# Kernel optimization log

Hardware: AMD Instinct MI355X
Metric: run time of the kernel (lower is better)

## Reference

```python
import jax, jax.numpy as jnp
import numpy as np

B, N, E_PER = 32, 2048, 16384
DIN, H = 128, 128
RATIO = 0.3


def setup_inputs() -> dict:
    key = jax.random.key(0)
    ks = jax.random.split(key, 16)
    s_in = 1.0 / np.sqrt(DIN)
    s_h = 1.0 / np.sqrt(H)
    inp = {
        "x": jax.random.normal(ks[0], (B * N, DIN), dtype=jnp.float32),
        "edge_src": jax.random.randint(ks[1], (B, E_PER), 0, N, dtype=jnp.int32),
        "edge_dst": jax.random.randint(ks[2], (B, E_PER), 0, N, dtype=jnp.int32),
        # SAGEConv layer 1: lin_l (neighbor agg, with bias), lin_r (root, no bias)
        "Wl1": jax.random.normal(ks[3], (H, DIN), dtype=jnp.float32) * s_in,
        "bl1": jnp.zeros((H,), dtype=jnp.float32),
        "Wr1": jax.random.normal(ks[4], (H, DIN), dtype=jnp.float32) * s_in,
        # SAGEConv layer 2
        "Wl2": jax.random.normal(ks[5], (H, H), dtype=jnp.float32) * s_h,
        "bl2": jnp.zeros((H,), dtype=jnp.float32),
        "Wr2": jax.random.normal(ks[6], (H, H), dtype=jnp.float32) * s_h,
        # TopKPooling score weight
        "pool_w": jax.random.normal(ks[7], (H,), dtype=jnp.float32) * s_h,
        # classifier MLP
        "Wc1": jax.random.normal(ks[8], (H, H), dtype=jnp.float32) * s_h,
        "bc1": jnp.zeros((H,), dtype=jnp.float32),
        "Wc2": jax.random.normal(ks[9], (1, H), dtype=jnp.float32) * s_h,
        "bc2": jnp.zeros((1,), dtype=jnp.float32),
    }
    return inp


def _sage_conv(x, src, dst, n_total, Wl, bl, Wr):
    # mean-aggregate neighbor messages: msg flows src -> dst
    msg = x[src]                                                   # [E, D] gather
    agg = jax.ops.segment_sum(msg, dst, num_segments=n_total)      # [Nt, D]
    deg = jax.ops.segment_sum(jnp.ones_like(dst, dtype=x.dtype), dst,
                              num_segments=n_total)
    agg = agg / jnp.maximum(deg, 1.0)[:, None]
    return agg @ Wl.T + bl + x @ Wr.T


def _forward(x, edge_src, edge_dst, Wl1, bl1, Wr1, Wl2, bl2, Wr2,
             pool_w, Wc1, bc1, Wc2, bc2):
    n_total = x.shape[0]
    # offset per-graph node ids into the disjoint-union batch
    off = (jnp.arange(B, dtype=edge_src.dtype) * N)[:, None]
    src = (edge_src + off).reshape(-1)
    dst = (edge_dst + off).reshape(-1)

    x = jax.nn.relu(_sage_conv(x, src, dst, n_total, Wl1, bl1, Wr1))
    x = jax.nn.relu(_sage_conv(x, src, dst, n_total, Wl2, bl2, Wr2))

    # TopKPooling: score = tanh(x . w / ||w||); keep top ceil(ratio*N) per graph
    score = jnp.tanh(x @ pool_w / jnp.linalg.norm(pool_w))         # [Nt]
    k = int(np.ceil(RATIO * N))                                    # 615
    vals, idx = jax.lax.top_k(score.reshape(B, N), k)              # [B, k]
    xg = x.reshape(B, N, -1)
    x_sel = jnp.take_along_axis(xg, idx[..., None], axis=1)        # [B, k, H]
    x_sel = x_sel * vals[..., None]                                # gate by score

    # global mean pool over kept nodes, then MLP classifier
    emb = x_sel.mean(axis=1)                                       # [B, H]
    h = jax.nn.relu(emb @ Wc1.T + bc1)
    return (h @ Wc2.T + bc2).squeeze(-1)                           # [B]


def reference(x, edge_src, edge_dst, Wl1, bl1, Wr1, Wl2, bl2, Wr2,
              pool_w, Wc1, bc1, Wc2, bc2):
    return _forward(x, edge_src, edge_dst, Wl1, bl1, Wr1, Wl2, bl2, Wr2,
                    pool_w, Wc1, bc1, Wc2, bc2)
```

## Files before the change

kernel.cpp:

```cpp
#include <hip/hip_runtime.h>
#include <stdint.h>
#include <math.h>

#define NB    32
#define NNODE 2048
#define NT    (NB*NNODE)
#define EPB   16384
#define ETOT  (NB*EPB)
#define DF    128
#define KSEL  615
#define EMAX  512

typedef __attribute__((ext_vector_type(8))) short bf16x8;
typedef __attribute__((ext_vector_type(4))) float f32x4;

__device__ __forceinline__ unsigned short f2bf(float f){
  uint32_t u = __float_as_uint(f);
  u += 0x7FFFu + ((u>>16)&1u);
  return (unsigned short)(u>>16);
}
__device__ __forceinline__ void split2(float f, unsigned short& hi, unsigned short& lo){
  unsigned short h = f2bf(f);
  float fh = __uint_as_float(((uint32_t)h)<<16);
  hi = h;
  lo = f2bf(f - fh);
}
__device__ __forceinline__ uint32_t f2mono(float f){
  uint32_t u = __float_as_uint(f);
  return (u & 0x80000000u) ? ~u : (u | 0x80000000u);
}
__device__ __forceinline__ float mono2f(uint32_t m){
  uint32_t u = (m & 0x80000000u) ? (m ^ 0x80000000u) : ~m;
  return __uint_as_float(u);
}

__global__ void k_deg(const int* __restrict__ edst, uint32_t* __restrict__ deg,
                      const float* __restrict__ Wl1, const float* __restrict__ Wr1,
                      const float* __restrict__ Wl2, const float* __restrict__ Wr2,
                      unsigned short* __restrict__ Bpk){
  const int bid = blockIdx.x;
  if (bid < ETOT/256){
    int e = bid*256 + threadIdx.x;
    int g = e >> 14;
    atomicAdd(&deg[g*NNODE + edst[e]], 1u);
  } else {
    int tt = (bid - ETOT/256)*256 + threadIdx.x;
    int layer = tt >> 12;
    int t2 = tt & 4095;
    const float* Wl = layer ? Wl2 : Wl1;
    const float* Wr = layer ? Wr2 : Wr1;
    unsigned short* B = Bpk + (size_t)layer*65536;
    int lane = t2 & 63;
    int ct   = (t2>>6) & 7;
    int ks   = (t2>>9) & 7;
    int c  = ct*16 + (lane & 15);
    int k0 = ks*32 + ((lane>>4)<<3);
    size_t base = ((size_t)((ks*8+ct)*2)*64 + lane)*8;
    #pragma unroll
    for (int j=0;j<8;++j){
      int k = k0 + j;
      float v = (k < DF) ? Wl[c*DF + k] : Wr[c*DF + (k-DF)];
      unsigned short h, l; split2(v, h, l);
      B[base + j]       = h;
      B[base + 512 + j] = l;
    }
  }
}

__global__ __launch_bounds__(1024) void k_scan1(const uint32_t* __restrict__ deg,
                        uint32_t* __restrict__ rowptr, uint32_t* __restrict__ bsum){
  __shared__ uint32_t sh[1024];
  int t = threadIdx.x; int base = blockIdx.x*1024;
  uint32_t v = deg[base+t];
  sh[t] = v;
  for (int off=1; off<1024; off<<=1){
    __syncthreads();
    uint32_t a = (t>=off) ? sh[t-off] : 0u;
    __syncthreads();
    sh[t] += a;
  }
  rowptr[base+t] = sh[t] - v;
  if (t==1023) bsum[blockIdx.x] = sh[1023];
}

__global__ void k_scan2(uint32_t* __restrict__ bsum){
  __shared__ uint32_t sh[64];
  int t = threadIdx.x;
  uint32_t v = bsum[t]; sh[t] = v;
  for (int off=1; off<64; off<<=1){
    __syncthreads();
    uint32_t a = (t>=off) ? sh[t-off] : 0u;
    __syncthreads();
    sh[t] += a;
  }
  bsum[t] = sh[t] - v;
}

__global__ __launch_bounds__(1024) void k_scan3(uint32_t* __restrict__ rowptr,
                                                const uint32_t* __restrict__ bsum){
  int i = blockIdx.x*1024 + threadIdx.x;
  rowptr[i] += bsum[i>>10];
  if (i==0) rowptr[NT] = ETOT;
}

__global__ void k_scatter(const int* __restrict__ esrc, const int* __restrict__ edst,
                          const uint32_t* __restrict__ rowptr, uint32_t* __restrict__ deg,
                          int* __restrict__ col){
  int e = blockIdx.x*256 + threadIdx.x;
  int g = e >> 14;
  int d = g*NNODE + edst[e];
  int s = g*NNODE + esrc[e];
  uint32_t old = atomicSub(&deg[d], 1u);
  col[rowptr[d] + old - 1u] = s;
}

template<int LAYER>
__global__ __launch_bounds__(128, 4) void k_sage(
    const float* __restrict__ Xin, const uint32_t* __restrict__ rowptr,
    const int* __restrict__ col, const unsigned short* __restrict__ Bpk,
    const float* __restrict__ bias, float* __restrict__ OUT,
    const float* __restrict__ pw, float* __restrict__ scores)
{
  __shared__ float smemA[32][132];
  __shared__ int lcol[EMAX];
  __shared__ uint32_t lrpl[33];

  const int t = threadIdx.x;
  const int g = blockIdx.x & 31, jb = blockIdx.x >> 5;
  const int rowBase = g*NNODE + jb*32;

  const uint32_t e0 = rowptr[rowBase];
  if (t < 33) lrpl[t] = rowptr[rowBase + t] - e0;
  const int ecnt = (int)(rowptr[rowBase + 32] - e0);
  for (int i=t; i<ecnt && i<EMAX; i+=128) lcol[i] = col[e0+i];
  __syncthreads();

  {
    const int grp = t >> 5, c = t & 31;
    int cur = grp*8;
    const int curEnd = grp*8 + 8;
    f32x4 accv = {0.f,0.f,0.f,0.f};

    auto flushrow = [&](){
      uint32_t d = lrpl[cur+1] - lrpl[cur];
      float invd = 1.0f / (float)(d ? d : 1u);
      *(f32x4*)&smemA[cur][4*c] = accv * invd;
      accv = (f32x4){0.f,0.f,0.f,0.f};
      cur++;
    };

    const uint32_t kb = lrpl[grp*8], ke = lrpl[curEnd];
    auto run = [&](auto colAt){
      f32x4 v[8], w[8];
      #pragma unroll
      for (int j=0;j<8;++j){
        uint32_t kk = kb + j;
        int s = colAt(kk < ke ? kk : kb);
        v[j] = *(const f32x4*)(Xin + (size_t)s*DF + 4*c);
      }
      for (uint32_t k = kb; k < ke; k += 8){
        #pragma unroll
        for (int j=0;j<8;++j){
          uint32_t kk = k + 8 + j;
          int s = colAt(kk < ke ? kk : k);
          w[j] = *(const f32x4*)(Xin + (size_t)s*DF + 4*c);
        }
        #pragma unroll
        for (int j=0;j<8;++j){
          uint32_t kk = k + j;
          if (kk < ke){
            while (lrpl[cur+1] <= kk) flushrow();
            accv += v[j];
          }
        }
        #pragma unroll
        for (int j=0;j<8;++j) v[j] = w[j];
      }
    };
    if (kb < ke){
      if (ecnt <= EMAX) run([&](uint32_t k){ return lcol[k]; });
      else              run([&](uint32_t k){ return col[e0+k]; });
    }
    while (cur < curEnd) flushrow();
  }
  __syncthreads();

  const int l = t & 63, wid = t >> 6;
  const int q = l >> 4, c16 = l & 15;
  const int arow = rowBase + wid*16 + c16;

  f32x4 own[8];
  #pragma unroll
  for (int ks4=0; ks4<4; ++ks4){
    const float* s = Xin + (size_t)arow*DF + ks4*32 + q*8;
    own[ks4*2]   = *(const f32x4*)s;
    own[ks4*2+1] = *(const f32x4*)(s+4);
  }

  f32x4 acc[8];
  #pragma unroll
  for (int ct=0; ct<8; ++ct) acc[ct] = (f32x4){0.f,0.f,0.f,0.f};

  #pragma unroll
  for (int ks=0; ks<8; ++ks){
    f32x4 A0, A1;
    if (ks < 4){
      const float* s = &smemA[wid*16 + c16][ks*32 + q*8];
      A0 = *(const f32x4*)s; A1 = *(const f32x4*)(s+4);
    } else {
      A0 = own[(ks-4)*2]; A1 = own[(ks-4)*2+1];
    }
    float v[8] = {A0.x,A0.y,A0.z,A0.w,A1.x,A1.y,A1.z,A1.w};
    bf16x8 ahi, alo;
    #pragma unroll
    for (int j=0;j<8;++j){
      unsigned short h, lo_; split2(v[j], h, lo_);
      ahi[j] = (short)h; alo[j] = (short)lo_;
    }
    const unsigned short* bp = Bpk + (size_t)ks*8192 + l*8;
    #pragma unroll
    for (int ct=0; ct<8; ++ct){
      bf16x8 bhi = *(const bf16x8*)(bp + ct*1024);
      bf16x8 blo = *(const bf16x8*)(bp + ct*1024 + 512);
      acc[ct] = __builtin_amdgcn_mfma_f32_16x16x32_bf16(ahi, bhi, acc[ct], 0,0,0);
      acc[ct] = __builtin_amdgcn_mfma_f32_16x16x32_bf16(ahi, blo, acc[ct], 0,0,0);
      acc[ct] = __builtin_amdgcn_mfma_f32_16x16x32_bf16(alo, bhi, acc[ct], 0,0,0);
    }
  }

  const int rowOut = rowBase + wid*16;
  if constexpr (LAYER==1){
    #pragma unroll
    for (int ct=0; ct<8; ++ct){
      int c = ct*16 + c16;
      float bv = bias[c];
      #pragma unroll
      for (int r=0; r<4; ++r){
        int grow = rowOut + q*4 + r;
        OUT[(size_t)grow*DF + c] = fmaxf(acc[ct][r] + bv, 0.f);
      }
    }
  } else {
    float ov[8][4];
    float pwv[8];
    float n2 = 0.f;
    #pragma unroll
    for (int ct=0; ct<8; ++ct){ pwv[ct] = pw[ct*16 + c16]; n2 += pwv[ct]*pwv[ct]; }
    n2 += __shfl_xor(n2,8,16); n2 += __shfl_xor(n2,4,16);
    n2 += __shfl_xor(n2,2,16); n2 += __shfl_xor(n2,1,16);
    float nrm = sqrtf(n2);
    #pragma unroll
    for (int ct=0; ct<8; ++ct){
      int c = ct*16 + c16;
      float bv = bias[c];
      #pragma unroll
      for (int r=0; r<4; ++r){
        int grow = rowOut + q*4 + r;
        float o = fmaxf(acc[ct][r] + bv, 0.f);
        OUT[(size_t)grow*DF + c] = o;
        ov[ct][r] = o;
      }
    }
    #pragma unroll
    for (int r=0; r<4; ++r){
      float p = 0.f;
      #pragma unroll
      for (int ct=0; ct<8; ++ct) p += ov[ct][r]*pwv[ct];
      p += __shfl_xor(p,8,16); p += __shfl_xor(p,4,16);
      p += __shfl_xor(p,2,16); p += __shfl_xor(p,1,16);
      if (c16 == 0) scores[rowOut + q*4 + r] = tanhf(p/nrm);
    }
  }
}

__global__ __launch_bounds__(1024) void k_topk(
    const float* __restrict__ scores, const float* __restrict__ H,
    const float* __restrict__ Wc1, const float* __restrict__ bc1,
    const float* __restrict__ Wc2, const float* __restrict__ bc2,
    float* __restrict__ out)
{
  __shared__ uint32_t keys[NNODE];
  __shared__ uint32_t hist[64];
  __shared__ uint32_t wsum[16];
  __shared__ uint32_t sh_b, sh_rank, sh_cnt;
  __shared__ unsigned short selidx[KSEL+1];
  __shared__ float selval[KSEL+1];
  __shared__ float part[8*DF];
  __shared__ float emb[DF];
  __shared__ float hred[DF];

  const int t = threadIdx.x; const int b = blockIdx.x;
  const int lane = t & 63, wid = t >> 6;
  const float* sc = scores + b*NNODE;

  for (int i=t; i<NNODE; i+=1024) keys[i] = f2mono(sc[i]);
  __syncthreads();

  uint32_t prefix = 0, prefmask = 0, rank = KSEL, cntT = 0;
  #pragma unroll
  for (int lev=0; lev<6; ++lev){
    const int shift = (lev<5) ? (26 - 6*lev) : 0;
    const uint32_t bmask = (lev<5) ? 63u : 3u;
    if (t < 64) hist[t] = 0;
    __syncthreads();
    for (int i=t; i<NNODE; i+=1024){
      uint32_t k = keys[i];
      if ((k & prefmask) == prefix) atomicAdd(&hist[(k>>shift)&bmask], 1u);
    }
    __syncthreads();
    if (t < 64){
      uint32_t x = hist[t];
      #pragma unroll
      for (int off=1; off<64; off<<=1){
        uint32_t y = __shfl_down(x, off, 64);
        if (t + off < 64) x += y;
      }
      uint32_t above = __shfl_down(x, 1, 64);
      if (t == 63) above = 0;
      if (above < rank && rank <= x){
        sh_b = (uint32_t)t; sh_rank = rank - above; sh_cnt = x - above;
      }
    }
    __syncthreads();
    prefix |= (sh_b << shift);
    prefmask |= (bmask << shift);
    rank = sh_rank; cntT = sh_cnt;
    __syncthreads();
  }
  const uint32_t T = prefix;
  const uint32_t m = rank;

  uint32_t k0 = keys[2*t], k1 = keys[2*t+1];
  uint32_t eq0 = (k0 == T), eq1 = (k1 == T);
  uint32_t eqr0 = 0, eqr1 = 0;

  if (m != cntT){
    uint32_t v = eq0 + eq1, x = v;
    #pragma unroll
    for (int off=1; off<64; off<<=1){
      uint32_t y = __shfl_up(x, off, 64);
      if (lane >= off) x += y;
    }
    if (lane == 63) wsum[wid] = x;
    __syncthreads();
    if (wid == 0){
      uint32_t s = (lane < 16) ? wsum[lane] : 0;
      #pragma unroll
      for (int off=1; off<16; off<<=1){
        uint32_t y = __shfl_up(s, off, 64);
        if (lane >= off) s += y;
      }
      if (lane < 16) wsum[lane] = s;
    }
    __syncthreads();
    uint32_t excl = (wid ? wsum[wid-1] : 0) + x - v;
    eqr0 = excl; eqr1 = excl + eq0;
    __syncthreads();
  }

  uint32_t sel0 = (k0 > T) || (eq0 && eqr0 < m);
  uint32_t sel1 = (k1 > T) || (eq1 && eqr1 < m);
  {
    uint32_t v = sel0 + sel1, x = v;
    #pragma unroll
    for (int off=1; off<64; off<<=1){
      uint32_t y = __shfl_up(x, off, 64);
      if (lane >= off) x += y;
    }
    if (lane == 63) wsum[wid] = x;
    __syncthreads();
    if (wid == 0){
      uint32_t s = (lane < 16) ? wsum[lane] : 0;
      #pragma unroll
      for (int off=1; off<16; off<<=1){
        uint32_t y = __shfl_up(s, off, 64);
        if (lane >= off) s += y;
      }
      if (lane < 16) wsum[lane] = s;
    }
    __syncthreads();
    uint32_t excl = (wid ? wsum[wid-1] : 0) + x - v;
    if (sel0){ selidx[excl] = (unsigned short)(2*t);   selval[excl] = mono2f(k0); }
    if (sel1){ selidx[excl+sel0] = (unsigned short)(2*t+1); selval[excl+sel0] = mono2f(k1); }
  }
  __syncthreads();

  const int pg = t >> 7, f = t & (DF-1);
  const float* Hb = H + (size_t)b*NNODE*DF;
  float accv = 0.f;
  int s2 = pg;
  for (; s2+24 < KSEL; s2 += 32){
    int i0=selidx[s2], i1=selidx[s2+8], i2=selidx[s2+16], i3=selidx[s2+24];
    float w0=selval[s2], w1=selval[s2+8], w2=selval[s2+16], w3=selval[s2+24];
    float v0=Hb[(size_t)i0*DF+f], v1=Hb[(size_t)i1*DF+f],
          v2=Hb[(size_t)i2*DF+f], v3=Hb[(size_t)i3*DF+f];
    accv += w0*v0 + w1*v1 + w2*v2 + w3*v3;
  }
  for (; s2<KSEL; s2+=8) accv += selval[s2]*Hb[(size_t)selidx[s2]*DF+f];
  part[pg*DF + f] = accv;
  __syncthreads();
  if (t < DF){
    float e = 0.f;
    for (int g2=0; g2<8; ++g2) e += part[g2*DF + t];
    emb[t] = e / (float)KSEL;
  }
  __syncthreads();
  if (t < DF){
    float hv = bc1[t];
    const float* wr = Wc1 + t*DF;
    for (int f2=0; f2<DF; ++f2) hv = fmaf(emb[f2], wr[f2], hv);
    hred[t] = fmaxf(hv, 0.f) * Wc2[t];
  }
  __syncthreads();
  if (t == 0){
    float o = bc2[0];
    for (int c2=0; c2<DF; ++c2) o += hred[c2];
    out[b] = o;
  }
}

extern "C" void kernel_launch(void* const* d_in, const int* in_sizes, int n_in,
                              void* d_out, int out_size, void* d_ws, size_t ws_size,
                              hipStream_t stream)
{
  (void)in_sizes; (void)n_in; (void)out_size; (void)ws_size;
  const float* x   = (const float*)d_in[0];
  const int* esrc  = (const int*)d_in[1];
  const int* edst  = (const int*)d_in[2];
  const float* Wl1 = (const float*)d_in[3];
  const float* bl1 = (const float*)d_in[4];
  const float* Wr1 = (const float*)d_in[5];
  const float* Wl2 = (const float*)d_in[6];
  const float* bl2 = (const float*)d_in[7];
  const float* Wr2 = (const float*)d_in[8];
  const float* pw  = (const float*)d_in[9];
  const float* Wc1 = (const float*)d_in[10];
  const float* bc1 = (const float*)d_in[11];
  const float* Wc2 = (const float*)d_in[12];
  const float* bc2 = (const float*)d_in[13];
  float* out = (float*)d_out;

  char* ws = (char*)d_ws;
  float*    H1     = (float*)   (ws + 0);
  float*    H2     = (float*)   (ws + 33554432);
  uint32_t* deg    = (uint32_t*)(ws + 67108864);
  uint32_t* rowptr = (uint32_t*)(ws + 67371008);
  int*      col    = (int*)     (ws + 67633408);
  float*    scores = (float*)   (ws + 69730560);
  uint32_t* bsum   = (uint32_t*)(ws + 69992704);
  unsigned short* Bpk = (unsigned short*)(ws + 69992960);

  hipMemsetAsync(deg, 0, NT*sizeof(uint32_t), stream);

  k_deg    <<<ETOT/256 + 32, 256, 0, stream>>>(edst, deg, Wl1, Wr1, Wl2, Wr2, Bpk);
  k_scan1  <<<64, 1024, 0, stream>>>(deg, rowptr, bsum);
  k_scan2  <<<1, 64, 0, stream>>>(bsum);
  k_scan3  <<<64, 1024, 0, stream>>>(rowptr, bsum);
  k_scatter<<<ETOT/256, 256, 0, stream>>>(esrc, edst, rowptr, deg, col);

  k_sage<1><<<NT/32, 128, 0, stream>>>(x,  rowptr, col, Bpk,         bl1,
                                       H1, nullptr, nullptr);
  k_sage<2><<<NT/32, 128, 0, stream>>>(H1, rowptr, col, Bpk + 65536, bl2,
                                       H2, pw, scores);

  k_topk<<<NB, 1024, 0, stream>>>(scores, H2, Wc1, bc1, Wc2, bc2, out);
}
```

Baseline: 159.0 us.

## Split SAGE layer into LDS-staged aggregation kernel and separate MFMA combine kernel

Replaces the fused gather+GEMM SAGE kernel with two kernels. The first kernel stages a 16-feature slice of one graph's node features (128KB) in LDS, then performs CSR mean aggregation from LDS instead of random global gathers. The second kernel reads the aggregated and root features from global memory and runs the split-bf16 MFMA combine. The intent is to make the neighbor gather cheaper, at the cost of an extra global write and read of the aggregated tensor per layer. The aggregation kernel also has low occupancy and walks edges one at a time per thread, with serial col loads.

New measurement: 287.4 us. 80.8% more time.

```diff
diff --git a/kernel.cpp b/kernel.cpp
--- a/kernel.cpp
+++ b/kernel.cpp
@@ -9,7 +9,6 @@
 #define ETOT  (NB*EPB)
 #define DF    128
 #define KSEL  615
-#define EMAX  512
 
 typedef __attribute__((ext_vector_type(8))) short bf16x8;
 typedef __attribute__((ext_vector_type(4))) float f32x4;
@@ -114,87 +113,91 @@
   col[rowptr[d] + old - 1u] = s;
 }
 
+__global__ __launch_bounds__(512) void k_aggX(
+    const float* __restrict__ Xin, const uint32_t* __restrict__ rowptr,
+    const int* __restrict__ col, float* __restrict__ AGG)
+{
+  extern __shared__ float Xs[];
+  const int t = threadIdx.x;
+  const int g = blockIdx.x & 31, sl = blockIdx.x >> 5;
+  const int f0 = sl*16;
+  const int gbase = g*NNODE;
+
+  {
+    const float4* Xg = (const float4*)(Xin + (size_t)gbase*DF + f0);
+    #pragma unroll
+    for (int i=0;i<16;++i){
+      int idx = i*512 + t;
+      int row = idx >> 2, q = idx & 3;
+      float4 v = Xg[(size_t)row*32 + q];
+      *(float4*)&Xs[row*16 + q*4] = v;
+    }
+  }
+  __syncthreads();
+
+  const int sg = t >> 2, q = t & 3;
+  int cur = sg*16;
+  const int curEnd = cur + 16;
+  const uint32_t kb = rowptr[gbase + cur];
+  const uint32_t ke = rowptr[gbase + curEnd];
+  uint32_t rstart = kb;
+  uint32_t rnext  = rowptr[gbase + cur + 1];
+  f32x4 accv = {0.f,0.f,0.f,0.f};
+
+  auto flush = [&](){
+    uint32_t d = rnext - rstart;
+    float invd = 1.0f / (float)(d ? d : 1u);
+    *(f32x4*)(AGG + (size_t)(gbase+cur)*DF + f0 + q*4) = accv * invd;
+    accv = (f32x4){0.f,0.f,0.f,0.f};
+    cur++;
+    rstart = rnext;
+    rnext = (cur < curEnd) ? rowptr[gbase + cur + 1] : 0xFFFFFFFFu;
+  };
+
+  uint32_t e = kb;
+  if (e < ke){
+    int s = col[e] & (NNODE-1);
+    f32x4 vcur = *(const f32x4*)&Xs[s*16 + q*4];
+    while (true){
+      uint32_t e2 = e + 1;
+      f32x4 vnext = {0.f,0.f,0.f,0.f};
+      bool more = (e2 < ke);
+      if (more){
+        int s2 = col[e2] & (NNODE-1);
+        vnext = *(const f32x4*)&Xs[s2*16 + q*4];
+      }
+      while (rnext <= e) flush();
+      accv += vcur;
+      if (!more) break;
+      vcur = vnext; e = e2;
+    }
+  }
+  while (cur < curEnd) flush();
+}
+
 template<int LAYER>
-__global__ __launch_bounds__(128, 4) void k_sage(
-    const float* __restrict__ Xin, const uint32_t* __restrict__ rowptr,
-    const int* __restrict__ col, const unsigned short* __restrict__ Bpk,
-    const float* __restrict__ bias, float* __restrict__ OUT,
-    const float* __restrict__ pw, float* __restrict__ scores)
+__global__ __launch_bounds__(256) void k_comb(
+    const float* __restrict__ AGG, const float* __restrict__ Xin,
+    const unsigned short* __restrict__ Bpk, const float* __restrict__ bias,
+    float* __restrict__ OUT, const float* __restrict__ pw,
+    float* __restrict__ scores)
 {
-  __shared__ float smemA[32][132];
-  __shared__ int lcol[EMAX];
-  __shared__ uint32_t lrpl[33];
-
   const int t = threadIdx.x;
   const int g = blockIdx.x & 31, jb = blockIdx.x >> 5;
-  const int rowBase = g*NNODE + jb*32;
-
-  const uint32_t e0 = rowptr[rowBase];
-  if (t < 33) lrpl[t] = rowptr[rowBase + t] - e0;
-  const int ecnt = (int)(rowptr[rowBase + 32] - e0);
-  for (int i=t; i<ecnt && i<EMAX; i+=128) lcol[i] = col[e0+i];
-  __syncthreads();
-
-  {
-    const int grp = t >> 5, c = t & 31;
-    int cur = grp*8;
-    const int curEnd = grp*8 + 8;
-    f32x4 accv = {0.f,0.f,0.f,0.f};
-
-    auto flushrow = [&](){
-      uint32_t d = lrpl[cur+1] - lrpl[cur];
-      float invd = 1.0f / (float)(d ? d : 1u);
-      *(f32x4*)&smemA[cur][4*c] = accv * invd;
-      accv = (f32x4){0.f,0.f,0.f,0.f};
-      cur++;
-    };
-
-    const uint32_t kb = lrpl[grp*8], ke = lrpl[curEnd];
-    auto run = [&](auto colAt){
-      f32x4 v[8], w[8];
-      #pragma unroll
-      for (int j=0;j<8;++j){
-        uint32_t kk = kb + j;
-        int s = colAt(kk < ke ? kk : kb);
-        v[j] = *(const f32x4*)(Xin + (size_t)s*DF + 4*c);
-      }
-      for (uint32_t k = kb; k < ke; k += 8){
-        #pragma unroll
-        for (int j=0;j<8;++j){
-          uint32_t kk = k + 8 + j;
-          int s = colAt(kk < ke ? kk : k);
-          w[j] = *(const f32x4*)(Xin + (size_t)s*DF + 4*c);
-        }
-        #pragma unroll
-        for (int j=0;j<8;++j){
-          uint32_t kk = k + j;
-          if (kk < ke){
-            while (lrpl[cur+1] <= kk) flushrow();
-            accv += v[j];
-          }
-        }
-        #pragma unroll
-        for (int j=0;j<8;++j) v[j] = w[j];
-      }
-    };
-    if (kb < ke){
-      if (ecnt <= EMAX) run([&](uint32_t k){ return lcol[k]; });
-      else              run([&](uint32_t k){ return col[e0+k]; });
-    }
-    while (cur < curEnd) flushrow();
-  }
-  __syncthreads();
-
   const int l = t & 63, wid = t >> 6;
   const int q = l >> 4, c16 = l & 15;
+  const int rowBase = g*NNODE + jb*64;
   const int arow = rowBase + wid*16 + c16;
 
-  f32x4 own[8];
+  f32x4 aggv[8], own[8];
   #pragma unroll
   for (int ks4=0; ks4<4; ++ks4){
+    const float* a = AGG + (size_t)arow*DF + ks4*32 + q*8;
+    aggv[ks4*2]   = *(const f32x4*)a;
+    aggv[ks4*2+1] = *(const f32x4*)(a+4);
     const float* s = Xin + (size_t)arow*DF + ks4*32 + q*8;
-    own[ks4*2]   = *(const f32x4*)s;
-    own[ks4*2+1] = *(const f32x4*)(s+4);
+    own[ks4*2]    = *(const f32x4*)s;
+    own[ks4*2+1]  = *(const f32x4*)(s+4);
   }
 
   f32x4 acc[8];
@@ -203,13 +206,8 @@
 
   #pragma unroll
   for (int ks=0; ks<8; ++ks){
-    f32x4 A0, A1;
-    if (ks < 4){
-      const float* s = &smemA[wid*16 + c16][ks*32 + q*8];
-      A0 = *(const f32x4*)s; A1 = *(const f32x4*)(s+4);
-    } else {
-      A0 = own[(ks-4)*2]; A1 = own[(ks-4)*2+1];
-    }
+    f32x4 A0 = (ks<4) ? aggv[ks*2]   : own[(ks-4)*2];
+    f32x4 A1 = (ks<4) ? aggv[ks*2+1] : own[(ks-4)*2+1];
     float v[8] = {A0.x,A0.y,A0.z,A0.w,A1.x,A1.y,A1.z,A1.w};
     bf16x8 ahi, alo;
     #pragma unroll
@@ -443,12 +441,16 @@
   char* ws = (char*)d_ws;
   float*    H1     = (float*)   (ws + 0);
   float*    H2     = (float*)   (ws + 33554432);
-  uint32_t* deg    = (uint32_t*)(ws + 67108864);
-  uint32_t* rowptr = (uint32_t*)(ws + 67371008);
-  int*      col    = (int*)     (ws + 67633408);
-  float*    scores = (float*)   (ws + 69730560);
-  uint32_t* bsum   = (uint32_t*)(ws + 69992704);
-  unsigned short* Bpk = (unsigned short*)(ws + 69992960);
+  float*    AGG    = (float*)   (ws + 67108864);
+  uint32_t* deg    = (uint32_t*)(ws + 100663296);
+  uint32_t* rowptr = (uint32_t*)(ws + 100925440);
+  int*      col    = (int*)     (ws + 101187840);
+  float*    scores = (float*)   (ws + 103284992);
+  uint32_t* bsum   = (uint32_t*)(ws + 103547136);
+  unsigned short* Bpk = (unsigned short*)(ws + 103547392);
+
+  (void)hipFuncSetAttribute((const void*)k_aggX,
+        hipFuncAttributeMaxDynamicSharedMemorySize, 131072);
 
   hipMemsetAsync(deg, 0, NT*sizeof(uint32_t), stream);
 
@@ -458,10 +460,12 @@
   k_scan3  <<<64, 1024, 0, stream>>>(rowptr, bsum);
   k_scatter<<<ETOT/256, 256, 0, stream>>>(esrc, edst, rowptr, deg, col);
 
-  k_sage<1><<<NT/32, 128, 0, stream>>>(x,  rowptr, col, Bpk,         bl1,
-                                       H1, nullptr, nullptr);
-  k_sage<2><<<NT/32, 128, 0, stream>>>(H1, rowptr, col, Bpk + 65536, bl2,
-                                       H2, pw, scores);
+  k_aggX   <<<256, 512, 131072, stream>>>(x,  rowptr, col, AGG);
+  k_comb<1><<<NT/64, 256, 0, stream>>>(AGG, x,  Bpk,         bl1, H1,
+                                       nullptr, nullptr);
+  k_aggX   <<<256, 512, 131072, stream>>>(H1, rowptr, col, AGG);
+  k_comb<2><<<NT/64, 256, 0, stream>>>(AGG, H1, Bpk + 65536, bl2, H2,
+                                       pw, scores);
 
   k_topk<<<NB, 1024, 0, stream>>>(scores, H2, Wc1, bc1, Wc2, bc2, out);
 }
```

## Use per-graph segmented scan and 16-bit local column indices

Applied to the files above, without the earlier changes.

Replaces the three-kernel global prefix scan with one kernel per graph that uses wave shuffles, relying on each graph having exactly EPB edges to set the offset g*EPB. Column indices are stored as 16-bit node ids local to each graph, and gathers use a per-graph base pointer. This removes two launches and halves the index traffic in scatter and aggregation. It assumes N fits in 16 bits and a fixed edge count per graph.

Result: faster. 153.2 us (median of 2 runs) (-3.6%).

```diff
diff --git a/kernel.cpp b/kernel.cpp
--- a/kernel.cpp
+++ b/kernel.cpp
@@ -4,8 +4,8 @@
 
 #define NB    32
 #define NNODE 2048
+#define EPB   16384
 #define NT    (NB*NNODE)
-#define EPB   16384
 #define ETOT  (NB*EPB)
 #define DF    128
 #define KSEL  615
@@ -67,72 +67,67 @@
   }
 }
 
-__global__ __launch_bounds__(1024) void k_scan1(const uint32_t* __restrict__ deg,
-                        uint32_t* __restrict__ rowptr, uint32_t* __restrict__ bsum){
-  __shared__ uint32_t sh[1024];
-  int t = threadIdx.x; int base = blockIdx.x*1024;
-  uint32_t v = deg[base+t];
-  sh[t] = v;
-  for (int off=1; off<1024; off<<=1){
-    __syncthreads();
-    uint32_t a = (t>=off) ? sh[t-off] : 0u;
-    __syncthreads();
-    sh[t] += a;
-  }
-  rowptr[base+t] = sh[t] - v;
-  if (t==1023) bsum[blockIdx.x] = sh[1023];
-}
-
-__global__ void k_scan2(uint32_t* __restrict__ bsum){
-  __shared__ uint32_t sh[64];
-  int t = threadIdx.x;
-  uint32_t v = bsum[t]; sh[t] = v;
+__global__ __launch_bounds__(256) void k_scanG(const uint32_t* __restrict__ deg,
+                                               uint32_t* __restrict__ rowptr){
+  __shared__ uint32_t wsum4[4];
+  const int g = blockIdx.x, t = threadIdx.x;
+  const int lane = t & 63, wid = t >> 6;
+  const uint32_t* dg = deg + g*NNODE;
+  uint32_t v[8]; const int b8 = t*8;
+  uint32_t tsum = 0;
+  #pragma unroll
+  for (int j=0;j<8;++j){ v[j] = dg[b8+j]; tsum += v[j]; }
+  uint32_t x = tsum;
+  #pragma unroll
   for (int off=1; off<64; off<<=1){
-    __syncthreads();
-    uint32_t a = (t>=off) ? sh[t-off] : 0u;
-    __syncthreads();
-    sh[t] += a;
-  }
-  bsum[t] = sh[t] - v;
-}
-
-__global__ __launch_bounds__(1024) void k_scan3(uint32_t* __restrict__ rowptr,
-                                                const uint32_t* __restrict__ bsum){
-  int i = blockIdx.x*1024 + threadIdx.x;
-  rowptr[i] += bsum[i>>10];
-  if (i==0) rowptr[NT] = ETOT;
+    uint32_t y = __shfl_up(x, off, 64);
+    if (lane >= off) x += y;
+  }
+  if (lane == 63) wsum4[wid] = x;
+  __syncthreads();
+  if (t == 0){
+    uint32_t a = 0;
+    #pragma unroll
+    for (int w=0; w<4; ++w){ uint32_t tmp=wsum4[w]; wsum4[w]=a; a+=tmp; }
+  }
+  __syncthreads();
+  uint32_t run = wsum4[wid] + x - tsum;
+  uint32_t* rp = rowptr + g*NNODE + b8;
+  #pragma unroll
+  for (int j=0;j<8;++j){ rp[j] = g*EPB + run; run += v[j]; }
+  if (g == 0 && t == 0) rowptr[NT] = ETOT;
 }
 
 __global__ void k_scatter(const int* __restrict__ esrc, const int* __restrict__ edst,
                           const uint32_t* __restrict__ rowptr, uint32_t* __restrict__ deg,
-                          int* __restrict__ col){
+                          unsigned short* __restrict__ colh){
   int e = blockIdx.x*256 + threadIdx.x;
   int g = e >> 14;
   int d = g*NNODE + edst[e];
-  int s = g*NNODE + esrc[e];
   uint32_t old = atomicSub(&deg[d], 1u);
-  col[rowptr[d] + old - 1u] = s;
+  colh[rowptr[d] + old - 1u] = (unsigned short)esrc[e];
 }
 
 template<int LAYER>
 __global__ __launch_bounds__(128, 4) void k_sage(
     const float* __restrict__ Xin, const uint32_t* __restrict__ rowptr,
-    const int* __restrict__ col, const unsigned short* __restrict__ Bpk,
+    const unsigned short* __restrict__ colh, const unsigned short* __restrict__ Bpk,
     const float* __restrict__ bias, float* __restrict__ OUT,
     const float* __restrict__ pw, float* __restrict__ scores)
 {
   __shared__ float smemA[32][132];
-  __shared__ int lcol[EMAX];
+  __shared__ unsigned short lcol[EMAX];
   __shared__ uint32_t lrpl[33];
 
   const int t = threadIdx.x;
   const int g = blockIdx.x & 31, jb = blockIdx.x >> 5;
   const int rowBase = g*NNODE + jb*32;
+  const float* Xg = Xin + (size_t)(g*NNODE)*DF;
 
   const uint32_t e0 = rowptr[rowBase];
   if (t < 33) lrpl[t] = rowptr[rowBase + t] - e0;
   const int ecnt = (int)(rowptr[rowBase + 32] - e0);
-  for (int i=t; i<ecnt && i<EMAX; i+=128) lcol[i] = col[e0+i];
+  for (int i=t; i<ecnt && i<EMAX; i+=128) lcol[i] = colh[e0+i];
   __syncthreads();
 
   {
@@ -156,14 +151,14 @@
       for (int j=0;j<8;++j){
         uint32_t kk = kb + j;
         int s = colAt(kk < ke ? kk : kb);
-        v[j] = *(const f32x4*)(Xin + (size_t)s*DF + 4*c);
+        v[j] = *(const f32x4*)(Xg + (size_t)s*DF + 4*c);
       }
       for (uint32_t k = kb; k < ke; k += 8){
         #pragma unroll
         for (int j=0;j<8;++j){
           uint32_t kk = k + 8 + j;
           int s = colAt(kk < ke ? kk : k);
-          w[j] = *(const f32x4*)(Xin + (size_t)s*DF + 4*c);
+          w[j] = *(const f32x4*)(Xg + (size_t)s*DF + 4*c);
         }
         #pragma unroll
         for (int j=0;j<8;++j){
@@ -178,8 +173,8 @@
       }
     };
     if (kb < ke){
-      if (ecnt <= EMAX) run([&](uint32_t k){ return lcol[k]; });
-      else              run([&](uint32_t k){ return col[e0+k]; });
+      if (ecnt <= EMAX) run([&](uint32_t k){ return (int)lcol[k]; });
+      else              run([&](uint32_t k){ return (int)colh[e0+k]; });
     }
     while (cur < curEnd) flushrow();
   }
@@ -445,22 +440,19 @@
   float*    H2     = (float*)   (ws + 33554432);
   uint32_t* deg    = (uint32_t*)(ws + 67108864);
   uint32_t* rowptr = (uint32_t*)(ws + 67371008);
-  int*      col    = (int*)     (ws + 67633408);
-  float*    scores = (float*)   (ws + 69730560);
-  uint32_t* bsum   = (uint32_t*)(ws + 69992704);
-  unsigned short* Bpk = (unsigned short*)(ws + 69992960);
+  unsigned short* colh = (unsigned short*)(ws + 67633408);
+  float*    scores = (float*)   (ws + 68681728);
+  unsigned short* Bpk = (unsigned short*)(ws + 68944128);
 
   hipMemsetAsync(deg, 0, NT*sizeof(uint32_t), stream);
 
   k_deg    <<<ETOT/256 + 32, 256, 0, stream>>>(edst, deg, Wl1, Wr1, Wl2, Wr2, Bpk);
-  k_scan1  <<<64, 1024, 0, stream>>>(deg, rowptr, bsum);
-  k_scan2  <<<1, 64, 0, stream>>>(bsum);
-  k_scan3  <<<64, 1024, 0, stream>>>(rowptr, bsum);
-  k_scatter<<<ETOT/256, 256, 0, stream>>>(esrc, edst, rowptr, deg, col);
-
-  k_sage<1><<<NT/32, 128, 0, stream>>>(x,  rowptr, col, Bpk,         bl1,
+  k_scanG  <<<NB, 256, 0, stream>>>(deg, rowptr);
+  k_scatter<<<ETOT/256, 256, 0, stream>>>(esrc, edst, rowptr, deg, colh);
+
+  k_sage<1><<<NT/32, 128, 0, stream>>>(x,  rowptr, colh, Bpk,         bl1,
                                        H1, nullptr, nullptr);
-  k_sage<2><<<NT/32, 128, 0, stream>>>(H1, rowptr, col, Bpk + 65536, bl2,
+  k_sage<2><<<NT/32, 128, 0, stream>>>(H1, rowptr, colh, Bpk + 65536, bl2,
                                        H2, pw, scores);
 
   k_topk<<<NB, 1024, 0, stream>>>(scores, H2, Wc1, bc1, Wc2, bc2, out);
```
